# Optimization experiments

Hardware: AMD Instinct MI355X
Metric: run time of the kernel (lower is better)

## Reference

```python
import jax, jax.numpy as jnp
import numpy as np
import math

H = 12  # heads (init kwarg)
KEEP_RATE = 0.7  # forward arg keep_rate (< 1 -> token pruning path)


def setup_inputs() -> dict:
    key = jax.random.key(0)
    k0, k1, k2 = jax.random.split(key, 3)
    b, n, c = 32, 577, 768  # ViT-B/16 @ 384px: 576 patches + CLS
    x = jax.random.normal(k0, (b, n, c), dtype=jnp.float32)
    # nn.Linear(dim, dim*3) and nn.Linear(dim, dim); kaiming-ish scale
    W_qkv = jax.random.normal(k1, (c, 3 * c), dtype=jnp.float32) / np.sqrt(c).astype(np.float32)
    b_qkv = jnp.zeros((3 * c,), dtype=jnp.float32)
    W_out = jax.random.normal(k2, (c, c), dtype=jnp.float32) / np.sqrt(c).astype(np.float32)
    b_out = jnp.zeros((c,), dtype=jnp.float32)
    return {"x": x, "keep_rate": KEEP_RATE, "W_qkv": W_qkv, "b_qkv": b_qkv,
            "W_out": W_out, "b_out": b_out}


def reference(x, keep_rate, W_qkv, b_qkv, W_out, b_out):
    b, n, c = x.shape
    d = c // H
    scale = (c / H) ** -0.5
    # qkv projection + split into heads: 'b n (h d) -> b h n d'
    qkv = x @ W_qkv + b_qkv                      # [b, n, 3c]
    q, k, v = jnp.split(qkv, 3, axis=-1)
    split_heads = lambda t: t.reshape(b, n, H, d).transpose(0, 2, 1, 3)
    q, k, v = split_heads(q), split_heads(k), split_heads(v)
    dots = jnp.einsum('bhid,bhjd->bhij', q, k) * scale   # [b,h,n,n]
    attention = jax.nn.softmax(dots, axis=-1)
    out = jnp.einsum('bhij,bhjd->bhid', attention, v)    # [b,h,n,d]
    out = out.transpose(0, 2, 1, 3).reshape(b, n, c)     # 'b h n d -> b n (h d)'
    out = out @ W_out + b_out                            # to_out (dropout=0)
    final_tokens = n - 1
    if keep_rate < 1:
        final_tokens = math.ceil(keep_rate * final_tokens)
        # CLS-token attention to patch tokens, averaged over heads
        class_attention = attention[:, :, 0, 1:].mean(axis=1)   # [b, n-1]
        _, ind = jax.lax.top_k(class_attention, final_tokens)    # [b, final_tokens]
        ind = jnp.sort(ind, axis=1)
        index = jnp.broadcast_to(ind[:, :, None], (b, final_tokens, c))
        return (x, index, ind, class_attention, final_tokens)
    return (out, None, None, None, final_tokens)
```

## Files before the change

### kernel.cpp

```cpp
#include <hip/hip_runtime.h>
#include <math.h>

#define BATCH 32
#define NTOK 577
#define NPATCH 576
#define CDIM 768
#define HEADS 12
#define DHEAD 64
#define W3 2304
#define FT 404

#define WS_WTIL  24576
#define WS_DBIAS 319488
#define WS_DOTS  319872

#define O_X      0ULL
#define O_INDEX  14180352ULL
#define O_IND    24109056ULL
#define O_CA     24121984ULL
#define O_FT     24140416ULL

__global__ __launch_bounds__(256) void k_fold(const float* __restrict__ x,
                                              const float* __restrict__ W,
                                              const float* __restrict__ bq,
                                              float* __restrict__ wtil,
                                              float* __restrict__ dbias) {
    __shared__ float x0s[4 * CDIM];
    __shared__ float qs[4 * DHEAD];
    const int h = blockIdx.x, bg = blockIdx.y, tid = threadIdx.x;
    const int bg4 = bg * 4;
    {
        float4* d4 = (float4*)x0s;
        for (int i = tid; i < 4 * CDIM / 4; i += 256) {
            const int bl = i / 192, r = i - bl * 192;
            d4[i] = ((const float4*)(x + (size_t)(bg4 + bl) * NTOK * CDIM))[r];
        }
    }
    __syncthreads();
    {
        const int d = tid & 63, wv = tid >> 6;
        const float* Wq = W + h * DHEAD + d;
        const float* xrow = x0s + wv * CDIM;
        float acc = 0.f;
        #pragma unroll 16
        for (int c = 0; c < CDIM; c++) acc += xrow[c] * Wq[(size_t)c * W3];
        const float q = acc + bq[h * DHEAD + d];
        qs[wv * DHEAD + d] = q;
        float t = q * bq[CDIM + h * DHEAD + d];
        #pragma unroll
        for (int off = 32; off; off >>= 1) t += __shfl_down(t, off);
        if (d == 0) dbias[(bg4 + wv) * HEADS + h] = t;
    }
    __syncthreads();
    {
        const int bl = tid >> 6, ci = tid & 63;
        float4 q4[16];
        const float4* qp = (const float4*)(qs + bl * DHEAD);
        #pragma unroll
        for (int t2 = 0; t2 < 16; t2++) q4[t2] = qp[t2];
        float* wout = wtil + ((size_t)(bg4 + bl) * HEADS + h) * CDIM;
        #pragma unroll 2
        for (int k = 0; k < 12; k++) {
            const int c = ci + k * 64;
            const float4* wr = (const float4*)(W + (size_t)c * W3 + CDIM + h * DHEAD);
            float acc = 0.f;
            #pragma unroll
            for (int t2 = 0; t2 < 16; t2++) {
                const float4 ww = wr[t2];
                acc += ww.x * q4[t2].x + ww.y * q4[t2].y + ww.z * q4[t2].z + ww.w * q4[t2].w;
            }
            wout[c] = acc;
        }
    }
}

__global__ __launch_bounds__(256) void k_dots(const float* __restrict__ x,
                                              const float* __restrict__ wtil,
                                              const float* __restrict__ dbias,
                                              float* __restrict__ dots,
                                              float* __restrict__ out0) {
    __shared__ float wt[HEADS * CDIM];
    __shared__ float db[HEADS];
    const int b = blockIdx.x, tid = threadIdx.x;
    for (int i = tid; i < HEADS * CDIM; i += 256) wt[i] = wtil[(size_t)b * HEADS * CDIM + i];
    if (tid < HEADS) db[tid] = dbias[b * HEADS + tid];
    __syncthreads();
    const int wave = tid >> 6, lane = tid & 63;
    for (int it = 0; it < 8; it++) {
        const int j = blockIdx.y * 32 + it * 4 + wave;
        if (j >= NTOK) break;
        const float4* xp = reinterpret_cast<const float4*>(x + ((size_t)b * NTOK + j) * CDIM);
        float4* op = reinterpret_cast<float4*>(out0 + ((size_t)b * NTOK + j) * CDIM);
        float acc[HEADS];
        #pragma unroll
        for (int h = 0; h < HEADS; h++) acc[h] = 0.f;
        #pragma unroll
        for (int i = 0; i < 3; i++) {
            float4 a = xp[i * 64 + lane];
            op[i * 64 + lane] = a;
            const int cbase = i * 256 + lane * 4;
            #pragma unroll
            for (int h = 0; h < HEADS; h++) {
                float4 w = *reinterpret_cast<const float4*>(&wt[h * CDIM + cbase]);
                acc[h] += a.x * w.x + a.y * w.y + a.z * w.z + a.w * w.w;
            }
        }
        #pragma unroll
        for (int off = 32; off; off >>= 1)
            #pragma unroll
            for (int h = 0; h < HEADS; h++) acc[h] += __shfl_xor(acc[h], off);
        if (lane == 0) {
            #pragma unroll
            for (int h = 0; h < HEADS; h++)
                dots[((size_t)b * HEADS + h) * NTOK + j] = 0.125f * (acc[h] + db[h]);
        }
    }
}

__global__ __launch_bounds__(256) void k_catbc(const float* __restrict__ dots,
                                               float* __restrict__ out,
                                               int write_ft) {
    __shared__ float dl[HEADS * NTOK];
    __shared__ float mh[HEADS], sh[HEADS];
    __shared__ unsigned vals[NPATCH];
    __shared__ unsigned long long segmask[9];
    __shared__ int segoff[9];
    __shared__ int ind_lds[FT];
    const int b = blockIdx.x, y = blockIdx.y, tid = threadIdx.x;
    {
        const float4* s4 = (const float4*)(dots + (size_t)b * HEADS * NTOK);
        float4* d4 = (float4*)dl;
        for (int i = tid; i < HEADS * NTOK / 4; i += 256) d4[i] = s4[i];
    }
    __syncthreads();
    const int w = tid >> 6, lane = tid & 63;
    #pragma unroll
    for (int hh = 0; hh < 3; hh++) {
        const int h = w * 3 + hh;
        const float* row = dl + h * NTOK;
        float m = -3.4e38f;
        for (int j = lane; j < NTOK; j += 64) m = fmaxf(m, row[j]);
        #pragma unroll
        for (int off = 32; off; off >>= 1) m = fmaxf(m, __shfl_xor(m, off));
        float s = 0.f;
        for (int j = lane; j < NTOK; j += 64) s += expf(row[j] - m);
        #pragma unroll
        for (int off = 32; off; off >>= 1) s += __shfl_xor(s, off);
        if (lane == 0) { mh[h] = m; sh[h] = s; }
    }
    __syncthreads();
    for (int t = tid; t < NPATCH; t += 256) {
        float ca = 0.f;
        #pragma unroll
        for (int h = 0; h < HEADS; h++)
            ca += expf(dl[h * NTOK + 1 + t] - mh[h]) / sh[h];
        ca *= (1.f / 12.f);
        if (y == 0) out[O_CA + (size_t)b * NPATCH + t] = ca;
        vals[t] = __float_as_uint(ca);
    }
    __syncthreads();
    {
        const uint4* v4 = (const uint4*)vals;
        for (int s = w; s < 9; s += 4) {
            const int t = s * 64 + lane;
            const unsigned myv = vals[t];
            int rank = 0;
            #pragma unroll 4
            for (int j4 = 0; j4 < NPATCH / 4; j4++) {
                const uint4 vv = v4[j4];
                const int j = j4 * 4;
                rank += (vv.x > myv) || (vv.x == myv && j     < t);
                rank += (vv.y > myv) || (vv.y == myv && j + 1 < t);
                rank += (vv.z > myv) || (vv.z == myv && j + 2 < t);
                rank += (vv.w > myv) || (vv.w == myv && j + 3 < t);
            }
            const unsigned long long mask = __ballot(rank < FT);
            if (lane == 0) segmask[s] = mask;
        }
    }
    __syncthreads();
    if (tid == 0) {
        int acc = 0;
        #pragma unroll
        for (int s = 0; s < 9; s++) { segoff[s] = acc; acc += __popcll(segmask[s]); }
    }
    __syncthreads();
    for (int s = w; s < 9; s += 4) {
        const int t = s * 64 + lane;
        const unsigned long long mask = segmask[s];
        if ((mask >> lane) & 1ull) {
            const int pos = segoff[s] + __popcll(mask & ((1ull << lane) - 1ull));
            ind_lds[pos] = t;
            if (y == 0) out[O_IND + (size_t)b * FT + pos] = (float)t;
        }
    }
    if (y == 0 && b == 0 && tid == 0 && write_ft) out[O_FT] = (float)FT;
    __syncthreads();
    {
        const int nrows = (FT - 1 - y) / 8 + 1;
        const int total = nrows * 192;
        for (int f = tid; f < total; f += 256) {
            const int k = f / 192, cc = f - k * 192;
            const int r = y + k * 8;
            const float v = (float)ind_lds[r];
            float4 o; o.x = v; o.y = v; o.z = v; o.w = v;
            ((float4*)(out + O_INDEX + ((size_t)b * FT + r) * CDIM))[cc] = o;
        }
    }
}

extern "C" void kernel_launch(void* const* d_in, const int* in_sizes, int n_in,
                              void* d_out, int out_size, void* d_ws, size_t ws_size,
                              hipStream_t stream) {
    const float* x  = (const float*)d_in[0];
    const float* W  = (const float*)d_in[2];
    const float* bq = (const float*)d_in[3];
    float* ws = (float*)d_ws;
    float* out = (float*)d_out;

    k_fold<<<dim3(HEADS, 8), 256, 0, stream>>>(x, W, bq, ws + WS_WTIL, ws + WS_DBIAS);
    k_dots<<<dim3(BATCH, 19), 256, 0, stream>>>(x, ws + WS_WTIL, ws + WS_DBIAS,
                                                ws + WS_DOTS, out + O_X);
    const int write_ft = (out_size > (int)O_FT) ? 1 : 0;
    k_catbc<<<dim3(BATCH, 8), 256, 0, stream>>>(ws + WS_DOTS, out, write_ft);
}
```

Baseline: 279.0 us.

## Repartition fold, dots and index-broadcast kernels for more parallelism

```diff
diff --git a/kernel.cpp b/kernel.cpp
--- a/kernel.cpp
+++ b/kernel.cpp
@@ -20,57 +20,49 @@
 #define O_CA     24121984ULL
 #define O_FT     24140416ULL
 
-__global__ __launch_bounds__(256) void k_fold(const float* __restrict__ x,
+__global__ __launch_bounds__(512) void k_fold(const float* __restrict__ x,
                                               const float* __restrict__ W,
                                               const float* __restrict__ bq,
                                               float* __restrict__ wtil,
                                               float* __restrict__ dbias) {
-    __shared__ float x0s[4 * CDIM];
-    __shared__ float qs[4 * DHEAD];
-    const int h = blockIdx.x, bg = blockIdx.y, tid = threadIdx.x;
-    const int bg4 = bg * 4;
-    {
-        float4* d4 = (float4*)x0s;
-        for (int i = tid; i < 4 * CDIM / 4; i += 256) {
-            const int bl = i / 192, r = i - bl * 192;
-            d4[i] = ((const float4*)(x + (size_t)(bg4 + bl) * NTOK * CDIM))[r];
-        }
-    }
-    __syncthreads();
-    {
-        const int d = tid & 63, wv = tid >> 6;
+    __shared__ float x0s[CDIM];
+    __shared__ float red[512];
+    __shared__ float qs[DHEAD];
+    const int b = blockIdx.x, h = blockIdx.y, tid = threadIdx.x;
+    if (tid < CDIM / 4)
+        ((float4*)x0s)[tid] = ((const float4*)(x + (size_t)b * NTOK * CDIM))[tid];
+    __syncthreads();
+    {
+        const int d = tid & 63, seg = tid >> 6;
         const float* Wq = W + h * DHEAD + d;
-        const float* xrow = x0s + wv * CDIM;
+        const int c0 = seg * 96;
         float acc = 0.f;
-        #pragma unroll 16
-        for (int c = 0; c < CDIM; c++) acc += xrow[c] * Wq[(size_t)c * W3];
-        const float q = acc + bq[h * DHEAD + d];
-        qs[wv * DHEAD + d] = q;
-        float t = q * bq[CDIM + h * DHEAD + d];
+        #pragma unroll 32
+        for (int c = c0; c < c0 + 96; c++) acc += x0s[c] * Wq[(size_t)c * W3];
+        red[tid] = acc;
+    }
+    __syncthreads();
+    if (tid < DHEAD) {
+        float q = red[tid];
+        #pragma unroll
+        for (int s = 1; s < 8; s++) q += red[tid + s * 64];
+        q += bq[h * DHEAD + tid];
+        qs[tid] = q;
+        float t = q * bq[CDIM + h * DHEAD + tid];
         #pragma unroll
         for (int off = 32; off; off >>= 1) t += __shfl_down(t, off);
-        if (d == 0) dbias[(bg4 + wv) * HEADS + h] = t;
-    }
-    __syncthreads();
-    {
-        const int bl = tid >> 6, ci = tid & 63;
-        float4 q4[16];
-        const float4* qp = (const float4*)(qs + bl * DHEAD);
-        #pragma unroll
-        for (int t2 = 0; t2 < 16; t2++) q4[t2] = qp[t2];
-        float* wout = wtil + ((size_t)(bg4 + bl) * HEADS + h) * CDIM;
-        #pragma unroll 2
-        for (int k = 0; k < 12; k++) {
-            const int c = ci + k * 64;
-            const float4* wr = (const float4*)(W + (size_t)c * W3 + CDIM + h * DHEAD);
-            float acc = 0.f;
-            #pragma unroll
-            for (int t2 = 0; t2 < 16; t2++) {
-                const float4 ww = wr[t2];
-                acc += ww.x * q4[t2].x + ww.y * q4[t2].y + ww.z * q4[t2].z + ww.w * q4[t2].w;
-            }
-            wout[c] = acc;
-        }
+        if (tid == 0) dbias[b * HEADS + h] = t;
+    }
+    __syncthreads();
+    for (int c = tid; c < CDIM; c += 512) {
+        const float* wr = W + (size_t)c * W3 + CDIM + h * DHEAD;
+        float acc = 0.f;
+        #pragma unroll
+        for (int d = 0; d < DHEAD; d += 4) {
+            float4 a = *reinterpret_cast<const float4*>(wr + d);
+            acc += a.x * qs[d] + a.y * qs[d + 1] + a.z * qs[d + 2] + a.w * qs[d + 3];
+        }
+        wtil[((size_t)b * HEADS + h) * CDIM + c] = acc;
     }
 }
 
@@ -79,45 +71,56 @@
                                               const float* __restrict__ dbias,
                                               float* __restrict__ dots,
                                               float* __restrict__ out0) {
-    __shared__ float wt[HEADS * CDIM];
-    __shared__ float db[HEADS];
     const int b = blockIdx.x, tid = threadIdx.x;
-    for (int i = tid; i < HEADS * CDIM; i += 256) wt[i] = wtil[(size_t)b * HEADS * CDIM + i];
-    if (tid < HEADS) db[tid] = dbias[b * HEADS + tid];
-    __syncthreads();
-    const int wave = tid >> 6, lane = tid & 63;
-    for (int it = 0; it < 8; it++) {
-        const int j = blockIdx.y * 32 + it * 4 + wave;
+    const int w = tid >> 6, lane = tid & 63, h0 = w * 3;
+    float4 wr[3][3];
+    float db[3];
+    #pragma unroll
+    for (int hh = 0; hh < 3; hh++) {
+        #pragma unroll
+        for (int i = 0; i < 3; i++)
+            wr[hh][i] = *reinterpret_cast<const float4*>(
+                wtil + ((size_t)b * HEADS + h0 + hh) * CDIM + i * 256 + lane * 4);
+        db[hh] = dbias[b * HEADS + h0 + hh];
+    }
+    const int jbase = blockIdx.y * 32;
+    for (int jj = 0; jj < 32; jj++) {
+        const int j = jbase + jj;
         if (j >= NTOK) break;
         const float4* xp = reinterpret_cast<const float4*>(x + ((size_t)b * NTOK + j) * CDIM);
-        float4* op = reinterpret_cast<float4*>(out0 + ((size_t)b * NTOK + j) * CDIM);
-        float acc[HEADS];
-        #pragma unroll
-        for (int h = 0; h < HEADS; h++) acc[h] = 0.f;
-        #pragma unroll
-        for (int i = 0; i < 3; i++) {
-            float4 a = xp[i * 64 + lane];
-            op[i * 64 + lane] = a;
-            const int cbase = i * 256 + lane * 4;
-            #pragma unroll
-            for (int h = 0; h < HEADS; h++) {
-                float4 w = *reinterpret_cast<const float4*>(&wt[h * CDIM + cbase]);
-                acc[h] += a.x * w.x + a.y * w.y + a.z * w.z + a.w * w.w;
-            }
-        }
+        const float4 a0 = xp[lane], a1 = xp[64 + lane], a2 = xp[128 + lane];
+        if (w == 0) {
+            float4* op = reinterpret_cast<float4*>(out0 + ((size_t)b * NTOK + j) * CDIM);
+            op[lane] = a0; op[64 + lane] = a1; op[128 + lane] = a2;
+        }
+        float acc[3];
+        #pragma unroll
+        for (int hh = 0; hh < 3; hh++) acc[hh] = 0.f;
+        #pragma unroll
+        for (int hh = 0; hh < 3; hh++)
+            acc[hh] += a0.x * wr[hh][0].x + a0.y * wr[hh][0].y
+                     + a0.z * wr[hh][0].z + a0.w * wr[hh][0].w;
+        #pragma unroll
+        for (int hh = 0; hh < 3; hh++)
+            acc[hh] += a1.x * wr[hh][1].x + a1.y * wr[hh][1].y
+                     + a1.z * wr[hh][1].z + a1.w * wr[hh][1].w;
+        #pragma unroll
+        for (int hh = 0; hh < 3; hh++)
+            acc[hh] += a2.x * wr[hh][2].x + a2.y * wr[hh][2].y
+                     + a2.z * wr[hh][2].z + a2.w * wr[hh][2].w;
         #pragma unroll
         for (int off = 32; off; off >>= 1)
             #pragma unroll
-            for (int h = 0; h < HEADS; h++) acc[h] += __shfl_xor(acc[h], off);
+            for (int hh = 0; hh < 3; hh++) acc[hh] += __shfl_xor(acc[hh], off);
         if (lane == 0) {
             #pragma unroll
-            for (int h = 0; h < HEADS; h++)
-                dots[((size_t)b * HEADS + h) * NTOK + j] = 0.125f * (acc[h] + db[h]);
-        }
-    }
-}
-
-__global__ __launch_bounds__(256) void k_catbc(const float* __restrict__ dots,
+            for (int hh = 0; hh < 3; hh++)
+                dots[((size_t)b * HEADS + h0 + hh) * NTOK + j] = 0.125f * (acc[hh] + db[hh]);
+        }
+    }
+}
+
+__global__ __launch_bounds__(512) void k_catbc(const float* __restrict__ dots,
                                                float* __restrict__ out,
                                                int write_ft) {
     __shared__ float dl[HEADS * NTOK];
@@ -130,13 +133,11 @@
     {
         const float4* s4 = (const float4*)(dots + (size_t)b * HEADS * NTOK);
         float4* d4 = (float4*)dl;
-        for (int i = tid; i < HEADS * NTOK / 4; i += 256) d4[i] = s4[i];
+        for (int i = tid; i < HEADS * NTOK / 4; i += 512) d4[i] = s4[i];
     }
     __syncthreads();
     const int w = tid >> 6, lane = tid & 63;
-    #pragma unroll
-    for (int hh = 0; hh < 3; hh++) {
-        const int h = w * 3 + hh;
+    for (int h = w; h < HEADS; h += 8) {
         const float* row = dl + h * NTOK;
         float m = -3.4e38f;
         for (int j = lane; j < NTOK; j += 64) m = fmaxf(m, row[j]);
@@ -149,7 +150,7 @@
         if (lane == 0) { mh[h] = m; sh[h] = s; }
     }
     __syncthreads();
-    for (int t = tid; t < NPATCH; t += 256) {
+    for (int t = tid; t < NPATCH; t += 512) {
         float ca = 0.f;
         #pragma unroll
         for (int h = 0; h < HEADS; h++)
@@ -161,11 +162,11 @@
     __syncthreads();
     {
         const uint4* v4 = (const uint4*)vals;
-        for (int s = w; s < 9; s += 4) {
+        for (int s = w; s < 9; s += 8) {
             const int t = s * 64 + lane;
             const unsigned myv = vals[t];
             int rank = 0;
-            #pragma unroll 4
+            #pragma unroll 8
             for (int j4 = 0; j4 < NPATCH / 4; j4++) {
                 const uint4 vv = v4[j4];
                 const int j = j4 * 4;
@@ -185,7 +186,7 @@
         for (int s = 0; s < 9; s++) { segoff[s] = acc; acc += __popcll(segmask[s]); }
     }
     __syncthreads();
-    for (int s = w; s < 9; s += 4) {
+    for (int s = w; s < 9; s += 8) {
         const int t = s * 64 + lane;
         const unsigned long long mask = segmask[s];
         if ((mask >> lane) & 1ull) {
@@ -197,11 +198,11 @@
     if (y == 0 && b == 0 && tid == 0 && write_ft) out[O_FT] = (float)FT;
     __syncthreads();
     {
-        const int nrows = (FT - 1 - y) / 8 + 1;
+        const int nrows = (FT - 1 - y) / 16 + 1;
         const int total = nrows * 192;
-        for (int f = tid; f < total; f += 256) {
+        for (int f = tid; f < total; f += 512) {
             const int k = f / 192, cc = f - k * 192;
-            const int r = y + k * 8;
+            const int r = y + k * 16;
             const float v = (float)ind_lds[r];
             float4 o; o.x = v; o.y = v; o.z = v; o.w = v;
             ((float4*)(out + O_INDEX + ((size_t)b * FT + r) * CDIM))[cc] = o;
@@ -218,9 +219,9 @@
     float* ws = (float*)d_ws;
     float* out = (float*)d_out;
 
-    k_fold<<<dim3(HEADS, 8), 256, 0, stream>>>(x, W, bq, ws + WS_WTIL, ws + WS_DBIAS);
+    k_fold<<<dim3(BATCH, HEADS), 512, 0, stream>>>(x, W, bq, ws + WS_WTIL, ws + WS_DBIAS);
     k_dots<<<dim3(BATCH, 19), 256, 0, stream>>>(x, ws + WS_WTIL, ws + WS_DBIAS,
                                                 ws + WS_DOTS, out + O_X);
     const int write_ft = (out_size > (int)O_FT) ? 1 : 0;
-    k_catbc<<<dim3(BATCH, 8), 256, 0, stream>>>(ws + WS_DOTS, out, write_ft);
-}
+    k_catbc<<<dim3(BATCH, 16), 512, 0, stream>>>(ws + WS_DOTS, out, write_ft);
+}
```

Result: faster. 246.8 us (-11.6%).
